# Optimization experiments

Measured on AMD Instinct MI355X. Metric: run time of the kernel, lower is better.

The kernel has to match this reference:

```python
import jax, jax.numpy as jnp
import numpy as np

B, N, D, TOP_K = 4, 4096, 256, 64
EPS = 1e-12  # F.normalize default eps


def setup_inputs() -> dict:
    key = jax.random.key(0)
    kx, kw, kb = jax.random.split(key, 3)
    x = jax.random.normal(kx, (B, N, D), dtype=jnp.float32)
    # value_fc: nn.Linear(in_dims, in_dims) -> weight [D, D], bias [D]
    lim = 1.0 / np.sqrt(D)
    W = jax.random.uniform(kw, (D, D), dtype=jnp.float32, minval=-lim, maxval=lim)
    b = jax.random.uniform(kb, (D,), dtype=jnp.float32, minval=-lim, maxval=lim)
    return {"x": x, "W": W, "b": b}


def reference(x, W, b):
    # value = value_fc(x)
    value = jnp.einsum("bnd,ed->bne", x, W) + b  # torch Linear: x @ W.T + b
    # F.normalize(x, p=2, dim=-1)
    norm = jnp.linalg.norm(x, axis=-1, keepdims=True)
    normed_x = x / jnp.maximum(norm, EPS)
    # full cosine-similarity matrix [B, N, N]
    cos_sim = jnp.einsum("bnd,bmd->bnm", normed_x, normed_x)
    # topk along last dim, scatter back into zeros
    topk_vals, topk_inds = jax.lax.top_k(cos_sim, TOP_K)  # [B, N, K]
    b_idx = jnp.arange(x.shape[0])[:, None, None]
    n_idx = jnp.arange(x.shape[1])[None, :, None]
    attn_sparse = jnp.zeros_like(cos_sim).at[b_idx, n_idx, topk_inds].set(topk_vals)
    # softmax over full row (zeros at non-topk positions contribute exp(0))
    attn = jax.nn.softmax(attn_sparse, axis=-1)
    return jnp.einsum("bnm,bmd->bnd", attn, value)
```

## Files before the change

### kernel.cpp

```cpp
#include <hip/hip_runtime.h>
#include <hip/hip_bf16.h>
#include <stdint.h>

#define B_ 4
#define N_ 4096
#define D_ 256
#define K_ 64
#define BN_ (B_*N_)

typedef __attribute__((ext_vector_type(8))) short bf16x8;
typedef __attribute__((ext_vector_type(8))) unsigned short u16x8;
typedef __attribute__((ext_vector_type(4))) float f32x4;

static __device__ __forceinline__ unsigned short f2bf(float f) {
  union { float f; unsigned u; } x; x.f = f;
  unsigned r = x.u + 0x7fffu + ((x.u >> 16) & 1u);
  return (unsigned short)(r >> 16);
}
static __device__ __forceinline__ float bf2f(unsigned short u) {
  union { unsigned u; float f; } x; x.u = ((unsigned)u) << 16;
  return x.f;
}
static __device__ __forceinline__ f32x4 mfma16(bf16x8 a, bf16x8 b, f32x4 c) {
  return __builtin_amdgcn_mfma_f32_16x16x32_bf16(a, b, c, 0, 0, 0);
}

__global__ __launch_bounds__(256) void prep_kernel(
    const float* __restrict__ x, const float* __restrict__ W,
    unsigned short* __restrict__ xn, float* __restrict__ norms,
    unsigned short* __restrict__ Wb, float* __restrict__ vsum) {
  const int bid = blockIdx.x;
  if (bid < 4096) {
    int row = bid * 4 + (threadIdx.x >> 6);
    int lane = threadIdx.x & 63;
    const float4 v = reinterpret_cast<const float4*>(x + (size_t)row * D_)[lane];
    float ss = v.x*v.x + v.y*v.y + v.z*v.z + v.w*v.w;
    #pragma unroll
    for (int off = 32; off > 0; off >>= 1) ss += __shfl_xor(ss, off);
    float nrm = sqrtf(ss);
    float scale = 1.0f / fmaxf(nrm, 1e-12f);
    ushort4 o;
    o.x = f2bf(v.x * scale); o.y = f2bf(v.y * scale);
    o.z = f2bf(v.z * scale); o.w = f2bf(v.w * scale);
    reinterpret_cast<ushort4*>(xn + (size_t)row * D_)[lane] = o;
    if (lane == 0) norms[row] = nrm;
  } else if (bid < 4160) {
    int i = (bid - 4096) * 256 + threadIdx.x;
    float4 v = reinterpret_cast<const float4*>(W)[i];
    ushort4 o; o.x = f2bf(v.x); o.y = f2bf(v.y); o.z = f2bf(v.z); o.w = f2bf(v.w);
    reinterpret_cast<ushort4*>(Wb)[i] = o;
  } else {
    reinterpret_cast<float4*>(vsum)[threadIdx.x] = (float4){0.f, 0.f, 0.f, 0.f};
  }
}

__global__ __launch_bounds__(256, 3) void compute_kernel(
    const unsigned short* __restrict__ xn, const float* __restrict__ norms,
    const unsigned short* __restrict__ Wb, const float* __restrict__ bias,
    unsigned short* __restrict__ value, float* __restrict__ vsum,
    unsigned short* __restrict__ S) {
  __shared__ __attribute__((aligned(16))) unsigned char smem[33792];
  unsigned char* As = smem;
  unsigned char* Bs = smem + 16384;
  float* ns_s   = (float*)(smem + 32768);
  float* bias_s = (float*)(smem + 33280);

  const int t = threadIdx.x, lane = t & 63, w = t >> 6;
  const int l15 = lane & 15, qv = lane >> 4, rb = qv * 4;
  const int wr = w >> 1, wc = w & 1;
  const int x7 = l15 & 7;

  const unsigned short* Asrc;
  const unsigned short* Bsrc;
  int rbG, cb, batch = 0;
  const bool vmode = (blockIdx.x < 256);
  if (vmode) {
    rbG = (blockIdx.x >> 1) * 128;
    cb  = (blockIdx.x & 1) * 128;
    Asrc = xn + (size_t)rbG * D_;
    Bsrc = Wb + (size_t)cb * D_;
    if (t < 128) { ns_s[t] = norms[rbG + t]; bias_s[t] = bias[cb + t]; }
  } else {
    int g = blockIdx.x - 256;
    batch = g >> 10;
    int tl = g & 1023;
    rbG = (tl >> 5) * 128;
    cb  = (tl & 31) * 128;
    Asrc = xn + ((size_t)batch * N_ + rbG) * D_;
    Bsrc = xn + ((size_t)batch * N_ + cb)  * D_;
  }

  f32x4 acc[4][4];
  #pragma unroll
  for (int i = 0; i < 4; i++)
    #pragma unroll
    for (int j = 0; j < 4; j++) acc[i][j] = (f32x4){0.f,0.f,0.f,0.f};

  for (int kk = 0; kk < 4; kk++) {
    #pragma unroll
    for (int p = 0; p < 4; p++) {
      int q = t + p * 256;
      int row = q >> 3, c = q & 7;
      int ld = row * 128 + ((c ^ (row & 7)) << 4);
      *(u16x8*)(As + ld) = *(const u16x8*)(Asrc + (size_t)row * D_ + kk * 64 + c * 8);
      *(u16x8*)(Bs + ld) = *(const u16x8*)(Bsrc + (size_t)row * D_ + kk * 64 + c * 8);
    }
    __syncthreads();
    #pragma unroll
    for (int ks = 0; ks < 2; ks++) {
      const int cpos = (((ks * 4 + qv) ^ x7) << 4);
      bf16x8 a[4], bb[4];
      #pragma unroll
      for (int rt = 0; rt < 4; rt++)
        a[rt] = *(const bf16x8*)(As + (wr*64 + rt*16 + l15) * 128 + cpos);
      #pragma unroll
      for (int ct = 0; ct < 4; ct++)
        bb[ct] = *(const bf16x8*)(Bs + (wc*64 + ct*16 + l15) * 128 + cpos);
      #pragma unroll
      for (int rt = 0; rt < 4; rt++)
        #pragma unroll
        for (int ct = 0; ct < 4; ct++)
          acc[rt][ct] = mfma16(a[rt], bb[ct], acc[rt][ct]);
    }
    __syncthreads();
  }

  unsigned short* kbuf = (unsigned short*)smem;
  if (vmode) {
    float vpart[4] = {0.f, 0.f, 0.f, 0.f};
    #pragma unroll
    for (int rt = 0; rt < 4; rt++)
      #pragma unroll
      for (int ct = 0; ct < 4; ct++) {
        int col_l = wc*64 + ct*16 + l15;
        int swc = ((col_l & 7) | ((((col_l >> 3)) << 3)));
        #pragma unroll
        for (int reg = 0; reg < 4; reg++) {
          int row_l = wr*64 + rt*16 + rb + reg;
          float v = acc[rt][ct][reg] * ns_s[row_l] + bias_s[col_l];
          int pos = (col_l & 7) | ((((col_l >> 3) ^ (row_l & 7))) << 3);
          kbuf[row_l * 128 + pos] = f2bf(v);
          vpart[ct] += v;
        }
        (void)swc;
      }
    int b2 = rbG >> 12;
    #pragma unroll
    for (int ct = 0; ct < 4; ct++)
      atomicAdd(&vsum[b2*D_ + cb + wc*64 + ct*16 + l15], vpart[ct]);
    __syncthreads();
    #pragma unroll
    for (int p = 0; p < 8; p++) {
      int q = t + p * 256;
      int row = q >> 4, c8 = q & 15;
      u16x8 d = *(const u16x8*)(kbuf + row * 128 + ((c8 ^ (row & 7)) << 3));
      *(u16x8*)(value + (size_t)(rbG + row) * D_ + cb + c8 * 8) = d;
    }
  } else {
    #pragma unroll
    for (int rt = 0; rt < 4; rt++)
      #pragma unroll
      for (int ct = 0; ct < 4; ct++) {
        int col_l = wc*64 + ct*16 + l15;
        #pragma unroll
        for (int reg = 0; reg < 4; reg++) {
          int row_l = wr*64 + rt*16 + rb + reg;
          unsigned short bits = f2bf(acc[rt][ct][reg]);
          unsigned short key = (bits & 0x8000u) ? (unsigned short)(~bits)
                                                : (unsigned short)(bits | 0x8000u);
          int pos = (col_l & 7) | ((((col_l >> 3) ^ (row_l & 7))) << 3);
          kbuf[row_l * 128 + pos] = key;
        }
      }
    __syncthreads();
    unsigned short* Sb = S + ((size_t)batch << 24);
    #pragma unroll
    for (int p = 0; p < 8; p++) {
      int q = t + p * 256;
      int row = q >> 4, c8 = q & 15;
      u16x8 d = *(const u16x8*)(kbuf + row * 128 + ((c8 ^ (row & 7)) << 3));
      *(u16x8*)(Sb + (size_t)(rbG + row) * N_ + cb + c8 * 8) = d;
    }
  }
}

__global__ __launch_bounds__(256, 4) void select_kernel(
    const unsigned short* __restrict__ S,
    const unsigned short* __restrict__ value,
    const float* __restrict__ vsum,
    float* __restrict__ out) {
  __shared__ __attribute__((aligned(16))) unsigned bb[4 * 2048];
  __shared__ unsigned wt4[4];
  __shared__ float zred[4];
  __shared__ int hb_s, cg_s, lb_s, cglo_s, nsel_s, neq_s;
  __shared__ int widx_s[64];
  __shared__ float wv_s[64];
  __shared__ float partial[4][256];

  const int t = threadIdx.x, lane = t & 63, w = t >> 6;
  const int b = blockIdx.x >> 12;
  const int r = blockIdx.x & 4095;
  const unsigned short* srow = S + ((size_t)b << 24) + ((size_t)r << 12);

  u16x8 va = *(const u16x8*)(srow + t*16);
  u16x8 vb2 = *(const u16x8*)(srow + t*16 + 8);
  unsigned ov[16];
  #pragma unroll
  for (int j = 0; j < 8; j++) { ov[j] = (unsigned short)va[j]; ov[j+8] = (unsigned short)vb2[j]; }

  #pragma unroll
  for (int p = 0; p < 8; p++)
    *(uint4*)&bb[(t + p*256)*4] = (uint4){0u,0u,0u,0u};
  if (t == 0) { nsel_s = 0; neq_s = 0; }
  __syncthreads();
  #pragma unroll
  for (int j = 0; j < 16; j++) atomicAdd(&bb[w*2048 + (ov[j] >> 5)], 1u);
  __syncthreads();
  unsigned cnt[8];
  #pragma unroll
  for (int j = 0; j < 8; j++) cnt[j] = 0;
  #pragma unroll
  for (int ww = 0; ww < 4; ww++) {
    uint4 c0 = *(const uint4*)&bb[ww*2048 + t*8];
    uint4 c1 = *(const uint4*)&bb[ww*2048 + t*8 + 4];
    cnt[0]+=c0.x; cnt[1]+=c0.y; cnt[2]+=c0.z; cnt[3]+=c0.w;
    cnt[4]+=c1.x; cnt[5]+=c1.y; cnt[6]+=c1.z; cnt[7]+=c1.w;
  }
  unsigned own = cnt[0]+cnt[1]+cnt[2]+cnt[3]+cnt[4]+cnt[5]+cnt[6]+cnt[7];
  unsigned v = own;
  #pragma unroll
  for (int off = 1; off < 64; off <<= 1) {
    unsigned o = __shfl_down(v, off);
    if (lane + off < 64) v += o;
  }
  if (lane == 0) wt4[w] = v;
  __syncthreads();
  unsigned sfx = v;
  #pragma unroll
  for (int ww = 0; ww < 4; ww++) if (ww > w) sfx += wt4[ww];
  unsigned nxt = sfx - own;
  if (sfx >= 64u && nxt < 64u) {
    unsigned c = nxt;
    #pragma unroll
    for (int jj = 7; jj >= 0; jj--) {
      unsigned cn = c + cnt[jj];
      if (cn >= 64u && c < 64u) { hb_s = t*8 + jj; cg_s = (int)c; }
      c = cn;
    }
  }
  if (t < 128) bb[(t >> 5)*2048 + (t & 31)] = 0;
  __syncthreads();
  const unsigned hb = (unsigned)hb_s;
  const unsigned need2 = (unsigned)(64 - cg_s);
  #pragma unroll
  for (int j = 0; j < 16; j++)
    if ((ov[j] >> 5) == hb) atomicAdd(&bb[w*2048 + (ov[j] & 31u)], 1u);
  __syncthreads();
  if (w == 0) {
    unsigned own2 = 0;
    if (lane < 32)
      own2 = bb[lane] + bb[2048 + lane] + bb[4096 + lane] + bb[6144 + lane];
    unsigned v2 = own2;
    #pragma unroll
    for (int off = 1; off < 64; off <<= 1) {
      unsigned o = __shfl_down(v2, off);
      if (lane + off < 64) v2 += o;
    }
    unsigned nxt2 = v2 - own2;
    if (lane < 32 && v2 >= need2 && nxt2 < need2) { lb_s = lane; cglo_s = (int)nxt2; }
  }
  __syncthreads();
  const unsigned tau = (hb << 5) | (unsigned)lb_s;
  const int needeq = (int)need2 - cglo_s;

  float zloc = 0.f;
  #pragma unroll
  for (int j = 0; j < 16; j++) {
    unsigned u = ov[j];
    bool take = (u > tau);
    if (!take && u == tau) { int k = atomicAdd(&neq_s, 1); take = (k < needeq); }
    if (take) {
      int slot = atomicAdd(&nsel_s, 1);
      unsigned short bits = (u & 0x8000u) ? (unsigned short)(u & 0x7FFFu)
                                          : (unsigned short)(~u);
      float s = bf2f(bits);
      float e = __expf(s);
      zloc += e;
      widx_s[slot] = t*16 + j;
      wv_s[slot] = e - 1.0f;
    }
  }
  #pragma unroll
  for (int off = 32; off > 0; off >>= 1) zloc += __shfl_xor(zloc, off);
  if (lane == 0) zred[w] = zloc;
  __syncthreads();
  const float Z = zred[0] + zred[1] + zred[2] + zred[3] + (float)(N_ - K_);

  const size_t vbase = (size_t)b << 20;
  float ax = 0.f, ay = 0.f, az = 0.f, aw = 0.f;
  #pragma unroll
  for (int i = 0; i < 16; i++) {
    int sel = w*16 + i;
    int idx = widx_s[sel];
    float wt = wv_s[sel];
    ushort4 vv = *reinterpret_cast<const ushort4*>(&value[vbase + (size_t)idx*D_ + lane*4]);
    ax += wt * bf2f(vv.x);
    ay += wt * bf2f(vv.y);
    az += wt * bf2f(vv.z);
    aw += wt * bf2f(vv.w);
  }
  partial[w][lane*4 + 0] = ax;
  partial[w][lane*4 + 1] = ay;
  partial[w][lane*4 + 2] = az;
  partial[w][lane*4 + 3] = aw;
  __syncthreads();
  float ps = partial[0][t] + partial[1][t] + partial[2][t] + partial[3][t];
  out[(((size_t)b << 12) + r) * D_ + t] = (ps + vsum[b*D_ + t]) * (1.0f / Z);
}

extern "C" void kernel_launch(void* const* d_in, const int* in_sizes, int n_in,
                              void* d_out, int out_size, void* d_ws, size_t ws_size,
                              hipStream_t stream) {
  const float* x    = (const float*)d_in[0];
  const float* W    = (const float*)d_in[1];
  const float* bias = (const float*)d_in[2];
  float* out = (float*)d_out;
  char* ws = (char*)d_ws;
  unsigned short* xn    = (unsigned short*)(ws);
  unsigned short* Wb    = (unsigned short*)(ws + 8388608);
  float*          norms = (float*)(ws + 8519680);
  unsigned short* value = (unsigned short*)(ws + 8585216);
  float*          vsum  = (float*)(ws + 16973824);
  unsigned short* S     = (unsigned short*)(ws + 16977920);

  prep_kernel<<<4161, 256, 0, stream>>>(x, W, xn, norms, Wb, vsum);
  compute_kernel<<<4352, 256, 0, stream>>>(xn, norms, Wb, bias, value, vsum, S);
  select_kernel<<<BN_, 256, 0, stream>>>(S, value, vsum, out);
}
```

Measured before the change: 249.1 us.

## Use direct global-to-LDS loads in GEMM and halve select-kernel LDS for occupancy

The GEMM tile loads now use global_load_lds, so data goes straight from global memory into shared memory with the XOR swizzle moved to the source address instead of passing through registers. In the select kernel the four per-wave histograms become two, each shared by a pair of waves, and the partial-sum buffer now reuses the histogram storage. This cuts LDS per block so 8 blocks per CU can be requested instead of 4. The cost is more atomic contention on the shared histograms, and the direct-to-LDS path depends on the swizzle mapping staying consistent with the reads.

```diff
diff --git a/kernel.cpp b/kernel.cpp
--- a/kernel.cpp
+++ b/kernel.cpp
@@ -11,6 +11,8 @@
 typedef __attribute__((ext_vector_type(8))) short bf16x8;
 typedef __attribute__((ext_vector_type(8))) unsigned short u16x8;
 typedef __attribute__((ext_vector_type(4))) float f32x4;
+typedef __attribute__((address_space(1))) const unsigned int gas_u32;
+typedef __attribute__((address_space(3))) unsigned int las_u32;
 
 static __device__ __forceinline__ unsigned short f2bf(float f) {
   union { float f; unsigned u; } x; x.f = f;
@@ -101,9 +103,13 @@
     for (int p = 0; p < 4; p++) {
       int q = t + p * 256;
       int row = q >> 3, c = q & 7;
-      int ld = row * 128 + ((c ^ (row & 7)) << 4);
-      *(u16x8*)(As + ld) = *(const u16x8*)(Asrc + (size_t)row * D_ + kk * 64 + c * 8);
-      *(u16x8*)(Bs + ld) = *(const u16x8*)(Bsrc + (size_t)row * D_ + kk * 64 + c * 8);
+      int cg = (c ^ (row & 7)) * 8;
+      __builtin_amdgcn_global_load_lds(
+          (gas_u32*)(Asrc + (size_t)row * D_ + kk * 64 + cg),
+          (las_u32*)(As + q * 16), 16, 0, 0);
+      __builtin_amdgcn_global_load_lds(
+          (gas_u32*)(Bsrc + (size_t)row * D_ + kk * 64 + cg),
+          (las_u32*)(Bs + q * 16), 16, 0, 0);
     }
     __syncthreads();
     #pragma unroll
@@ -133,7 +139,6 @@
       #pragma unroll
       for (int ct = 0; ct < 4; ct++) {
         int col_l = wc*64 + ct*16 + l15;
-        int swc = ((col_l & 7) | ((((col_l >> 3)) << 3)));
         #pragma unroll
         for (int reg = 0; reg < 4; reg++) {
           int row_l = wr*64 + rt*16 + rb + reg;
@@ -142,7 +147,6 @@
           kbuf[row_l * 128 + pos] = f2bf(v);
           vpart[ct] += v;
         }
-        (void)swc;
       }
     int b2 = rbG >> 12;
     #pragma unroll
@@ -184,20 +188,21 @@
   }
 }
 
-__global__ __launch_bounds__(256, 4) void select_kernel(
+__global__ __launch_bounds__(256, 8) void select_kernel(
     const unsigned short* __restrict__ S,
     const unsigned short* __restrict__ value,
     const float* __restrict__ vsum,
     float* __restrict__ out) {
-  __shared__ __attribute__((aligned(16))) unsigned bb[4 * 2048];
+  __shared__ __attribute__((aligned(16))) unsigned bb2[2][2048];
   __shared__ unsigned wt4[4];
   __shared__ float zred[4];
   __shared__ int hb_s, cg_s, lb_s, cglo_s, nsel_s, neq_s;
   __shared__ int widx_s[64];
   __shared__ float wv_s[64];
-  __shared__ float partial[4][256];
+  float* partial = (float*)bb2;
 
   const int t = threadIdx.x, lane = t & 63, w = t >> 6;
+  const int cp = w >> 1;
   const int b = blockIdx.x >> 12;
   const int r = blockIdx.x & 4095;
   const unsigned short* srow = S + ((size_t)b << 24) + ((size_t)r << 12);
@@ -209,22 +214,21 @@
   for (int j = 0; j < 8; j++) { ov[j] = (unsigned short)va[j]; ov[j+8] = (unsigned short)vb2[j]; }
 
   #pragma unroll
-  for (int p = 0; p < 8; p++)
-    *(uint4*)&bb[(t + p*256)*4] = (uint4){0u,0u,0u,0u};
+  for (int p = 0; p < 4; p++)
+    *(uint4*)&bb2[0][(t + p*256)*4] = (uint4){0u,0u,0u,0u};
   if (t == 0) { nsel_s = 0; neq_s = 0; }
   __syncthreads();
   #pragma unroll
-  for (int j = 0; j < 16; j++) atomicAdd(&bb[w*2048 + (ov[j] >> 5)], 1u);
+  for (int j = 0; j < 16; j++) atomicAdd(&bb2[cp][ov[j] >> 5], 1u);
   __syncthreads();
   unsigned cnt[8];
-  #pragma unroll
-  for (int j = 0; j < 8; j++) cnt[j] = 0;
-  #pragma unroll
-  for (int ww = 0; ww < 4; ww++) {
-    uint4 c0 = *(const uint4*)&bb[ww*2048 + t*8];
-    uint4 c1 = *(const uint4*)&bb[ww*2048 + t*8 + 4];
-    cnt[0]+=c0.x; cnt[1]+=c0.y; cnt[2]+=c0.z; cnt[3]+=c0.w;
-    cnt[4]+=c1.x; cnt[5]+=c1.y; cnt[6]+=c1.z; cnt[7]+=c1.w;
+  {
+    uint4 c0 = *(const uint4*)&bb2[0][t*8];
+    uint4 c1 = *(const uint4*)&bb2[0][t*8 + 4];
+    uint4 d0 = *(const uint4*)&bb2[1][t*8];
+    uint4 d1 = *(const uint4*)&bb2[1][t*8 + 4];
+    cnt[0]=c0.x+d0.x; cnt[1]=c0.y+d0.y; cnt[2]=c0.z+d0.z; cnt[3]=c0.w+d0.w;
+    cnt[4]=c1.x+d1.x; cnt[5]=c1.y+d1.y; cnt[6]=c1.z+d1.z; cnt[7]=c1.w+d1.w;
   }
   unsigned own = cnt[0]+cnt[1]+cnt[2]+cnt[3]+cnt[4]+cnt[5]+cnt[6]+cnt[7];
   unsigned v = own;
@@ -248,18 +252,17 @@
       c = cn;
     }
   }
-  if (t < 128) bb[(t >> 5)*2048 + (t & 31)] = 0;
+  if (t < 64) bb2[t >> 5][t & 31] = 0;
   __syncthreads();
   const unsigned hb = (unsigned)hb_s;
   const unsigned need2 = (unsigned)(64 - cg_s);
   #pragma unroll
   for (int j = 0; j < 16; j++)
-    if ((ov[j] >> 5) == hb) atomicAdd(&bb[w*2048 + (ov[j] & 31u)], 1u);
+    if ((ov[j] >> 5) == hb) atomicAdd(&bb2[cp][ov[j] & 31u], 1u);
   __syncthreads();
   if (w == 0) {
     unsigned own2 = 0;
-    if (lane < 32)
-      own2 = bb[lane] + bb[2048 + lane] + bb[4096 + lane] + bb[6144 + lane];
+    if (lane < 32) own2 = bb2[0][lane] + bb2[1][lane];
     unsigned v2 = own2;
     #pragma unroll
     for (int off = 1; off < 64; off <<= 1) {
@@ -309,12 +312,12 @@
     az += wt * bf2f(vv.z);
     aw += wt * bf2f(vv.w);
   }
-  partial[w][lane*4 + 0] = ax;
-  partial[w][lane*4 + 1] = ay;
-  partial[w][lane*4 + 2] = az;
-  partial[w][lane*4 + 3] = aw;
-  __syncthreads();
-  float ps = partial[0][t] + partial[1][t] + partial[2][t] + partial[3][t];
+  partial[w*256 + lane*4 + 0] = ax;
+  partial[w*256 + lane*4 + 1] = ay;
+  partial[w*256 + lane*4 + 2] = az;
+  partial[w*256 + lane*4 + 3] = aw;
+  __syncthreads();
+  float ps = partial[t] + partial[256 + t] + partial[512 + t] + partial[768 + t];
   out[(((size_t)b << 12) + r) * D_ + t] = (ps + vsum[b*D_ + t]) * (1.0f / Z);
 }
 
```

New measurement: 222.0 us. -10.9%, faster.
